# Performance work log

Measured on AMD Instinct MI355X. Metric: run time of the kernel, lower is better.

The kernel has to match this reference:

```python
import jax, jax.numpy as jnp
import numpy as np

B, C, H, W = 64, 256, 14, 14
K = 9
HID = 256   # EdgeAgg hidden_channels = in_channels
OUT = 512   # out_channels = 2*in_channels (required by final reshape)


def _knn(q, kset, k):
    # ViG dense_knn_matrix: squared-distance knn, top-k of -dist (self-loop may be included)
    qs = jnp.sum(q * q, -1)
    ks = jnp.sum(kset * kset, -1)
    dist = qs[:, :, None] - 2.0 * jnp.einsum('bnc,bmc->bnm', q, kset) + ks[:, None, :]
    _, idx = jax.lax.top_k(-dist, k)   # (B,N,k) neighbor indices into kset
    return idx


def _edgeconv_add(feat, nbr, validf, w, b):
    # PyG EdgeConv(nn=Linear, aggr='add') with per-node valid-edge mask:
    #   out[i] = sum_{j in valid nbrs(i)} cat(x_i, x_j - x_i) @ w + b
    # nn is linear, so aggregate neighbor diffs BEFORE the matmul (same math, less traffic).
    Cf = feat.shape[-1]
    wa, wb = w[:Cf], w[Cf:]
    deg = jnp.sum(validf, -1, keepdims=True)                   # (B,N,1)
    xj = feat[jnp.arange(feat.shape[0])[:, None, None], nbr]   # (B,N,k,C) gather
    sum_xj = jnp.einsum('bnkc,bnk->bnc', xj, validf)
    return deg * (feat @ wa + b) + (sum_xj - deg * feat) @ wb


def _forward(x, fc1_w, fc1_b, fc2_w, fc2_b, fce_w, fce_b, inout_w, inout_b,
             attn_w, attn_b, upd_w, upd_b, kp_w, kp_b, enc_w, enc_b,
             mu_w, mu_b, dec_w, dec_b, T):
    k = dec_w.shape[-1]
    b_, c_, h_, w_ = x.shape
    n = h_ * w_
    xs = x.reshape(b_, c_, n)                       # (B,C,N)
    x_sp = jnp.transpose(xs, (0, 2, 1))             # (B,N,C) true spatial node feats for knn
    x_sp_d = jax.lax.stop_gradient(x_sp)            # original detaches before knn
    x_nbr = _knn(x_sp_d, x_sp_d, k)
    # temporal roll across the T frames of each clip
    y_sp = jnp.roll(x_sp.reshape(b_ // T, T, n, c_), -1, axis=1).reshape(b_, n, c_)
    y_nbr = _knn(x_sp_d, jax.lax.stop_gradient(y_sp), k)
    # faithful to original: x.view(B*N, C) reinterprets the contiguous (B,C,N) buffer
    x_feat = xs.reshape(b_, n, c_)
    y_feat = jnp.transpose(y_sp, (0, 2, 1)).reshape(b_, n, c_)
    # VAE-like K predictor (deterministic z = mu); argmax -> per-node degree in [0,k)
    hk = x_feat.reshape(b_ * n, c_) @ kp_w + kp_b
    hk = jax.nn.relu(hk @ enc_w + enc_b)
    mu = hk @ mu_w + mu_b
    logits = mu @ dec_w + dec_b                     # (B*N, k)
    k_int = jnp.argmax(logits, axis=1)
    # generate_mask: keep the first k_int[i] of node i's k edges
    validf = (jnp.arange(k)[None, :] < k_int[:, None]).astype(x.dtype).reshape(b_, n, k)

    def edge_agg(feat, nbr):
        h1 = jax.nn.relu(_edgeconv_add(feat, nbr, validf, fc1_w, fc1_b))
        h2 = _edgeconv_add(h1, nbr, validf, fc2_w, fc2_b)
        return (h2 @ fce_w + fce_b).reshape(b_ * n, -1)

    x_agg = edge_agg(x_feat, x_nbr)
    y_agg = edge_agg(y_feat, y_nbr)
    scores = (jnp.concatenate([x_agg, y_agg], -1) @ attn_w + attn_b)[:, 0]
    wgt = jax.nn.softmax(scores, axis=0)[:, None]   # softmax over ALL B*N nodes (as in source)
    fused = wgt * x_agg + (1.0 - wgt) * y_agg
    xin = x_feat.reshape(b_ * n, c_) @ inout_w + inout_b
    upd = jax.nn.relu(jnp.concatenate([xin, fused], -1) @ upd_w + upd_b)   # (B*N, 2C)
    return jnp.transpose(upd.reshape(b_, n, 2 * c_), (0, 2, 1)).reshape(b_, 2 * c_, h_, w_)


def setup_inputs():
    key = jax.random.key(0)
    ks = iter(jax.random.split(key, 32))

    def lin(i, o):
        return jax.random.normal(next(ks), (i, o), jnp.float32) / np.sqrt(i)

    def bias(o):
        return jax.random.normal(next(ks), (o,), jnp.float32) * 0.01

    return {
        'x': jax.random.normal(next(ks), (B, C, H, W), jnp.float32),
        'fc1_w': lin(2 * C, HID), 'fc1_b': bias(HID),
        'fc2_w': lin(2 * HID, HID), 'fc2_b': bias(HID),
        'fce_w': lin(HID, OUT), 'fce_b': bias(OUT),
        'inout_w': lin(C, OUT), 'inout_b': bias(OUT),
        'attn_w': lin(2 * OUT, 1), 'attn_b': bias(1),
        'upd_w': lin(2 * OUT, OUT), 'upd_b': bias(OUT),
        'kp_w': lin(C, 500), 'kp_b': bias(500),
        'enc_w': lin(500, 64), 'enc_b': bias(64),
        'mu_w': lin(64, 32), 'mu_b': bias(32),
        'dec_w': lin(32, K), 'dec_b': bias(K),
        'T': 16,
    }


def reference(x, fc1_w, fc1_b, fc2_w, fc2_b, fce_w, fce_b, inout_w, inout_b,
              attn_w, attn_b, upd_w, upd_b, kp_w, kp_b, enc_w, enc_b,
              mu_w, mu_b, dec_w, dec_b, T):
    return _forward(x, fc1_w, fc1_b, fc2_w, fc2_b, fce_w, fce_b, inout_w, inout_b,
                    attn_w, attn_b, upd_w, upd_b, kp_w, kp_b, enc_w, enc_b,
                    mu_w, mu_b, dec_w, dec_b, T)
```

## Files before the change

### kernel.cpp

```cpp
#include <hip/hip_runtime.h>
#include <cstddef>
#include <cstdint>

constexpr int BATCH = 64;
constexpr int CH    = 256;
constexpr int NPT   = 196;
constexpr int ROWS  = BATCH * NPT;
constexpr int BSTRIDE = CH * NPT;
constexpr int KNB   = 8;
constexpr int DSTR  = 208;

typedef __bf16 bf16x8 __attribute__((ext_vector_type(8)));
typedef __bf16 bf16x4 __attribute__((ext_vector_type(4)));
typedef _Float16 f16x8 __attribute__((ext_vector_type(8)));
typedef float  f32x4  __attribute__((ext_vector_type(4)));
typedef unsigned long long u64;

__device__ __forceinline__ int src_batch(int b) {
    return (b & ~15) | ((b + 1) & 15);
}

__device__ __forceinline__ void gload_lds16(const void* g, void* l) {
    __builtin_amdgcn_global_load_lds(
        (const __attribute__((address_space(1))) void*)g,
        (__attribute__((address_space(3))) void*)l, 16, 0, 0);
}

__device__ __forceinline__ int xcd_swz(int lin, int nwg) {
    int q = nwg >> 3;
    return (lin & 7) * q + (lin >> 3);
}

__global__ __launch_bounds__(256) void front_kernel(const float* __restrict__ x,
        _Float16* __restrict__ XH, _Float16* __restrict__ XL,
        __bf16* __restrict__ XB, float* __restrict__ qs,
        const float* __restrict__ W1, const float* __restrict__ b1,
        const float* __restrict__ W2, const float* __restrict__ b2,
        int* __restrict__ kint, float* __restrict__ degf) {
    __shared__ __attribute__((aligned(16))) char smem[21056];
    int bid = blockIdx.x;
    int t = threadIdx.x;
    if (bid < 1024) {
        float (*tile)[65] = (float(*)[65])smem;
        int m0 = (bid & 3) * 64, c0 = ((bid >> 2) & 3) * 64, b = bid >> 4;
        const float* xb = x + (size_t)b * BSTRIDE;
        #pragma unroll
        for (int s = 0; s < 16; ++s) {
            int idx = s * 256 + t;
            int cc = idx >> 6, mm = idx & 63;
            int m = m0 + mm;
            float v = (m < NPT) ? xb[(size_t)(c0 + cc) * NPT + m] : 0.f;
            tile[cc][mm] = v;
            if (m < NPT)
                XB[(size_t)b * BSTRIDE + (size_t)(c0 + cc) * NPT + m] = (__bf16)v;
        }
        __syncthreads();
        #pragma unroll
        for (int s = 0; s < 16; ++s) {
            int idx = s * 256 + t;
            int mm = idx >> 6, cc = idx & 63;
            float v = tile[cc][mm];
            _Float16 h = (_Float16)v;
            size_t off = ((size_t)b * 256 + (m0 + mm)) * 256 + c0 + cc;
            XH[off] = h;
            XL[off] = (_Float16)(v - (float)h);
        }
    } else if (bid < 1088) {
        int b = bid - 1024;
        int m = t;
        if (m >= NPT) return;
        const float* xb = x + (size_t)b * BSTRIDE;
        float acc = 0.f;
        for (int c = 0; c < CH; ++c) {
            float v = xb[c * NPT + m];
            acc = fmaf(v, v, acc);
        }
        qs[b * NPT + m] = acc;
    } else {
        float (*xr)[256] = (float(*)[256])smem;
        float (*ebuf)[64] = (float(*)[64])(smem + 16384);
        float (*lg)[9]   = (float(*)[9])(smem + 20480);
        int r0 = (bid - 1088) * 16;
        const float4* xg = (const float4*)(x + (size_t)r0 * 256);
        float4* xs = (float4*)&xr[0][0];
        #pragma unroll
        for (int s = 0; s < 4; ++s) xs[s * 256 + t] = xg[s * 256 + t];
        __syncthreads();
        int w = t >> 6, l = t & 63;
        {
            float bb = b1[l];
            float a0 = bb, a1 = bb, a2 = bb, a3 = bb;
            const float* x0 = xr[w * 4 + 0];
            const float* x1 = xr[w * 4 + 1];
            const float* x2 = xr[w * 4 + 2];
            const float* x3 = xr[w * 4 + 3];
            for (int c = 0; c < 256; ++c) {
                float wv = W1[c * 64 + l];
                a0 = fmaf(x0[c], wv, a0);
                a1 = fmaf(x1[c], wv, a1);
                a2 = fmaf(x2[c], wv, a2);
                a3 = fmaf(x3[c], wv, a3);
            }
            ebuf[w * 4 + 0][l] = fmaxf(a0, 0.f);
            ebuf[w * 4 + 1][l] = fmaxf(a1, 0.f);
            ebuf[w * 4 + 2][l] = fmaxf(a2, 0.f);
            ebuf[w * 4 + 3][l] = fmaxf(a3, 0.f);
        }
        __syncthreads();
        int rr = t >> 4, cc = t & 15;
        if (cc < 9) {
            float acc = b2[cc];
            for (int j = 0; j < 64; ++j)
                acc = fmaf(ebuf[rr][j], W2[j * 9 + cc], acc);
            lg[rr][cc] = acc;
        }
        __syncthreads();
        if (cc == 0) {
            float best = lg[rr][0];
            int bi = 0;
            #pragma unroll
            for (int j = 1; j < 9; ++j)
                if (lg[rr][j] > best) { best = lg[rr][j]; bi = j; }
            kint[r0 + rr] = bi;
            degf[r0 + rr] = (float)bi;
        }
    }
}

__global__ __launch_bounds__(256) void gram_mfma(const _Float16* __restrict__ XH,
        const _Float16* __restrict__ XL, const float* __restrict__ qs,
        float* __restrict__ Dw) {
    __shared__ __attribute__((aligned(16))) _Float16 Ah[128 * 64];
    __shared__ __attribute__((aligned(16))) _Float16 Al[128 * 64];
    __shared__ __attribute__((aligned(16))) _Float16 Bh[128 * 64];
    __shared__ __attribute__((aligned(16))) _Float16 Bl[128 * 64];
    int lin = blockIdx.x + 2 * blockIdx.y + 4 * blockIdx.z;
    int nid = xcd_swz(lin, 512);
    int bx = nid & 1, by = (nid >> 1) & 1;
    int job = nid >> 2;
    int qb = (job < 64) ? job : job - 64;
    int kb = (job < 64) ? qb : src_batch(qb);
    int t = threadIdx.x, w = t >> 6, l = t & 63;
    int r0 = by * 128, c0 = bx * 128;
    int lr = l & 15, lg = l >> 4;
    int wr = (w >> 1) * 64, wc = (w & 1) * 64;
    const _Float16* qh = XH + (size_t)qb * 65536;
    const _Float16* ql = XL + (size_t)qb * 65536;
    const _Float16* kh = XH + (size_t)kb * 65536;
    const _Float16* kl = XL + (size_t)kb * 65536;
    f32x4 acc[4][4] = {};
    for (int k0 = 0; k0 < 256; k0 += 64) {
        #pragma unroll
        for (int i = 0; i < 4; ++i) {
            int row = (w * 4 + i) * 8 + (l >> 3);
            int c8 = l & 7;
            size_t goA = (size_t)(r0 + row) * 256 + k0 + c8 * 8;
            size_t goB = (size_t)(c0 + row) * 256 + k0 + c8 * 8;
            gload_lds16(qh + goA, Ah + (w * 4 + i) * 512);
            gload_lds16(ql + goA, Al + (w * 4 + i) * 512);
            gload_lds16(kh + goB, Bh + (w * 4 + i) * 512);
            gload_lds16(kl + goB, Bl + (w * 4 + i) * 512);
        }
        asm volatile("s_waitcnt vmcnt(0)" ::: "memory");
        __syncthreads();
        #pragma unroll
        for (int ks = 0; ks < 2; ++ks) {
            f16x8 ah[4], al[4], bh[4], bl[4];
            #pragma unroll
            for (int mi = 0; mi < 4; ++mi) {
                ah[mi] = *(const f16x8*)(Ah + (wr + mi * 16 + lr) * 64 + ks * 32 + lg * 8);
                al[mi] = *(const f16x8*)(Al + (wr + mi * 16 + lr) * 64 + ks * 32 + lg * 8);
            }
            #pragma unroll
            for (int ni = 0; ni < 4; ++ni) {
                bh[ni] = *(const f16x8*)(Bh + (wc + ni * 16 + lr) * 64 + ks * 32 + lg * 8);
                bl[ni] = *(const f16x8*)(Bl + (wc + ni * 16 + lr) * 64 + ks * 32 + lg * 8);
            }
            #pragma unroll
            for (int mi = 0; mi < 4; ++mi)
                #pragma unroll
                for (int ni = 0; ni < 4; ++ni) {
                    acc[mi][ni] = __builtin_amdgcn_mfma_f32_16x16x32_f16(
                        ah[mi], bh[ni], acc[mi][ni], 0, 0, 0);
                    acc[mi][ni] = __builtin_amdgcn_mfma_f32_16x16x32_f16(
                        ah[mi], bl[ni], acc[mi][ni], 0, 0, 0);
                    acc[mi][ni] = __builtin_amdgcn_mfma_f32_16x16x32_f16(
                        al[mi], bh[ni], acc[mi][ni], 0, 0, 0);
                }
        }
        __syncthreads();
    }
    const float* qsq = qs + qb * NPT;
    const float* qsk = qs + kb * NPT;
    float ksv[4];
    #pragma unroll
    for (int ni = 0; ni < 4; ++ni) {
        int col = c0 + wc + ni * 16 + lr;
        ksv[ni] = (col < NPT) ? qsk[col] : 0.f;
    }
    #pragma unroll
    for (int mi = 0; mi < 4; ++mi) {
        #pragma unroll
        for (int r = 0; r < 4; ++r) {
            if (r0 + wr + mi * 16 + r >= NPT) continue;
            int grow = r0 + wr + mi * 16 + lg * 4 + r;
            if (grow >= NPT) continue;
            float qq = qsq[grow];
            size_t rbase = ((size_t)job * NPT + grow) * DSTR;
            #pragma unroll
            for (int ni = 0; ni < 4; ++ni) {
                int col = c0 + wc + ni * 16 + lr;
                if (col < NPT)
                    Dw[rbase + col] = qq - 2.f * acc[mi][ni][r] + ksv[ni];
            }
        }
    }
}

__global__ __launch_bounds__(256) void topk_kernel(const float* __restrict__ Dw,
                                                   int* __restrict__ nbr) {
    __shared__ u64 lists[64][4][8];
    int t = threadIdx.x;
    int lrow = t >> 2, q = t & 3;
    int rowid = blockIdx.x * 64 + lrow;
    const float* rp = Dw + (size_t)rowid * DSTR + q * 52;
    u64 kreg[8];
    #pragma unroll
    for (int p = 0; p < 8; ++p) kreg[p] = ~0ull;
    for (int s4 = 0; s4 < 13; ++s4) {
        f32x4 dv = *(const f32x4*)(rp + s4 * 4);
        #pragma unroll
        for (int e = 0; e < 4; ++e) {
            int col = q * 52 + s4 * 4 + e;
            unsigned u = __float_as_uint(dv[e]);
            u = (u & 0x80000000u) ? ~u : (u | 0x80000000u);
            u64 key = (col < NPT) ? (((u64)u << 32) | (unsigned)col) : ~0ull;
            if (key < kreg[7]) {
                #pragma unroll
                for (int p = 0; p < 8; ++p) {
                    u64 mn = (key < kreg[p]) ? key : kreg[p];
                    u64 mx = (key < kreg[p]) ? kreg[p] : key;
                    kreg[p] = mn; key = mx;
                }
            }
        }
    }
    #pragma unroll
    for (int p = 0; p < 8; ++p) lists[lrow][q][p] = kreg[p];
    __syncthreads();
    if (q == 0) {
        const u64* c = &lists[lrow][0][0];
        int p0 = 0, p1 = 0, p2 = 0, p3 = 0;
        #pragma unroll
        for (int it = 0; it < 8; ++it) {
            u64 v0 = c[p0], v1 = c[8 + p1], v2 = c[16 + p2], v3 = c[24 + p3];
            u64 best = v0; int bj = 0;
            if (v1 < best) { best = v1; bj = 1; }
            if (v2 < best) { best = v2; bj = 2; }
            if (v3 < best) { best = v3; bj = 3; }
            if (bj == 0) p0 = (p0 < 7) ? p0 + 1 : 7;
            else if (bj == 1) p1 = (p1 < 7) ? p1 + 1 : 7;
            else if (bj == 2) p2 = (p2 < 7) ? p2 + 1 : 7;
            else p3 = (p3 < 7) ? p3 + 1 : 7;
            nbr[(size_t)rowid * KNB + it] = (int)(best & 0xffffffffu);
        }
    }
}

__global__ __launch_bounds__(256) void prep_weights(
        const float* __restrict__ fc1_w, const float* __restrict__ fc2_w,
        const float* __restrict__ fce_w, const float* __restrict__ upd_w,
        const float* __restrict__ kp_w, const float* __restrict__ kp_b,
        const float* __restrict__ enc_w, const float* __restrict__ enc_b,
        const float* __restrict__ mu_w, const float* __restrict__ mu_b,
        const float* __restrict__ dec_w, const float* __restrict__ dec_b,
        const float* __restrict__ inout_w, const float* __restrict__ inout_b,
        const float* __restrict__ upd_b,
        __bf16* __restrict__ W1catT, __bf16* __restrict__ W2catT,
        __bf16* __restrict__ fcet, __bf16* __restrict__ updC,
        float* __restrict__ KW1, float* __restrict__ kb1,
        float* __restrict__ KW2, float* __restrict__ kb2,
        float* __restrict__ bcomp) {
    __shared__ float tile[64][65];
    int bid = blockIdx.x;
    int t = threadIdx.x;
    if (bid < 64) {
        const float* W = (bid < 32) ? fc1_w : fc2_w;
        __bf16* WT = (bid < 32) ? W1catT : W2catT;
        int local = bid & 31;
        int n0 = (local >> 2) * 64, k0 = (local & 3) * 64;
        #pragma unroll
        for (int s = 0; s < 16; ++s) {
            int idx = s * 256 + t;
            int kk = idx >> 6, nn = idx & 63;
            float v;
            if (n0 < 256)
                v = W[(size_t)(k0 + kk) * 256 + n0 + nn] -
                    W[(size_t)(k0 + kk + 256) * 256 + n0 + nn];
            else
                v = W[(size_t)(k0 + kk + 256) * 256 + (n0 - 256) + nn];
            tile[kk][nn] = v;
        }
        __syncthreads();
        #pragma unroll
        for (int s = 0; s < 16; ++s) {
            int idx = s * 256 + t;
            int nn = idx >> 6, kk = idx & 63;
            WT[(size_t)(n0 + nn) * 256 + k0 + kk] = (__bf16)tile[kk][nn];
        }
    } else if (bid < 96) {
        int local = bid - 64;
        int n0 = (local >> 2) * 64, k0 = (local & 3) * 64;
        #pragma unroll
        for (int s = 0; s < 16; ++s) {
            int idx = s * 256 + t;
            int kk = idx >> 6, nn = idx & 63;
            tile[kk][nn] = fce_w[(size_t)(k0 + kk) * 512 + n0 + nn];
        }
        __syncthreads();
        #pragma unroll
        for (int s = 0; s < 16; ++s) {
            int idx = s * 256 + t;
            int nn = idx >> 6, kk = idx & 63;
            fcet[(size_t)(n0 + nn) * 256 + k0 + kk] = (__bf16)tile[kk][nn];
        }
    } else if (bid < 160) {
        int local = bid - 96;
        int k0 = (local >> 3) * 64, n0 = (local & 7) * 64;
        #pragma unroll
        for (int s = 0; s < 16; ++s) {
            int idx = s * 256 + t;
            int kk = idx >> 6, nn = idx & 63;
            tile[kk][nn] = upd_w[(size_t)(512 + k0 + kk) * 512 + n0 + nn];
        }
        __syncthreads();
        #pragma unroll
        for (int s = 0; s < 16; ++s) {
            int idx = s * 256 + t;
            int nn = idx >> 6, kk = idx & 63;
            updC[(size_t)(n0 + nn) * 768 + 256 + k0 + kk] = (__bf16)tile[kk][nn];
        }
    } else if (bid < 224) {
        int i = (bid - 160) * 4 + (t >> 6);
        int j = t & 63;
        double acc = 0.0;
        for (int k = 0; k < 500; ++k)
            acc += (double)kp_w[(size_t)i * 500 + k] * (double)enc_w[(size_t)k * 64 + j];
        KW1[i * 64 + j] = (float)acc;
    } else if (bid == 224) {
        int j = t;
        if (j < 64) {
            double acc = (double)enc_b[j];
            for (int k = 0; k < 500; ++k)
                acc += (double)kp_b[k] * (double)enc_w[(size_t)k * 64 + j];
            kb1[j] = (float)acc;
        }
    } else if (bid < 228) {
        int e = (bid - 225) * 256 + t;
        if (e < 576) {
            int i = e / 9, j = e - (e / 9) * 9;
            double acc = 0.0;
            for (int k = 0; k < 32; ++k)
                acc += (double)mu_w[(size_t)i * 32 + k] * (double)dec_w[(size_t)k * 9 + j];
            KW2[e] = (float)acc;
        } else if (e < 585) {
            int j = e - 576;
            double acc = (double)dec_b[j];
            for (int k = 0; k < 32; ++k)
                acc += (double)mu_b[k] * (double)dec_w[(size_t)k * 9 + j];
            kb2[j] = (float)acc;
        }
    } else if (bid < 740) {
        int e = (bid - 228) * 256 + t;
        int k = e >> 9, n = e & 511;
        double acc = 0.0;
        for (int j = 0; j < 512; ++j)
            acc += (double)inout_w[(size_t)k * 512 + j] * (double)upd_w[(size_t)j * 512 + n];
        updC[(size_t)n * 768 + k] = (__bf16)(float)acc;
    } else {
        int n = (bid - 740) * 256 + t;
        double acc = (double)upd_b[n];
        for (int j = 0; j < 512; ++j)
            acc += (double)inout_b[j] * (double)upd_w[(size_t)j * 512 + n];
        bcomp[n] = (float)acc;
    }
}

template<int STAGE, int RELU>
__global__ __launch_bounds__(256) void combine_kernel(const __bf16* __restrict__ P,
        const int* __restrict__ nbr, const int* __restrict__ kint_,
        const float* __restrict__ degf, const float* __restrict__ bias,
        __bf16* __restrict__ H) {
    int g = threadIdx.x >> 6, lane = threadIdx.x & 63;
    int nid = xcd_swz(blockIdx.x, 2 * ROWS / 4);
    int r = nid * 4 + g;
    int branch = (r >= ROWS);
    int rr = r - branch * ROWS;
    int b = rr / NPT, i = rr - b * NPT;
    size_t srow, mbase;
    if constexpr (STAGE == 1) {
        int fb = branch ? src_batch(b) : b;
        srow = (size_t)fb * NPT + i;
        mbase = (size_t)fb * NPT;
    } else {
        srow = (size_t)r;
        mbase = (size_t)branch * ROWS + (size_t)b * NPT;
    }
    const int* nb = nbr + (size_t)branch * ((size_t)ROWS * KNB) + (size_t)rr * KNB;
    bf16x4 sv = *(const bf16x4*)(P + srow * 512 + lane * 4);
    float4 bv = *(const float4*)(bias + lane * 4);
    float s0 = 0.f, s1 = 0.f, s2 = 0.f, s3 = 0.f;
    int kk = kint_[rr];
    for (int tt = 0; tt < kk; ++tt) {
        int m = nb[tt];
        bf16x4 v = *(const bf16x4*)(P + (mbase + m) * 512 + 256 + lane * 4);
        s0 += (float)v[0]; s1 += (float)v[1]; s2 += (float)v[2]; s3 += (float)v[3];
    }
    float dg = degf[rr];
    float o0 = fmaf(dg, (float)sv[0] + bv.x, s0);
    float o1 = fmaf(dg, (float)sv[1] + bv.y, s1);
    float o2 = fmaf(dg, (float)sv[2] + bv.z, s2);
    float o3 = fmaf(dg, (float)sv[3] + bv.w, s3);
    if constexpr (RELU) {
        o0 = fmaxf(o0, 0.f); o1 = fmaxf(o1, 0.f);
        o2 = fmaxf(o2, 0.f); o3 = fmaxf(o3, 0.f);
    }
    bf16x4 ov;
    ov[0] = (__bf16)o0; ov[1] = (__bf16)o1; ov[2] = (__bf16)o2; ov[3] = (__bf16)o3;
    *(bf16x4*)(H + (size_t)r * 256 + lane * 4) = ov;
}

template<int FLAGS, int CONCAT>
__global__ __launch_bounds__(256) void mfma_gemm(
    const __bf16* __restrict__ A0, const __bf16* __restrict__ A1,
    const __bf16* __restrict__ WT, const float* __restrict__ bias,
    float* __restrict__ Cf, __bf16* __restrict__ Cb, int K, int N,
    const float* __restrict__ aw, float* __restrict__ scp,
    const float* __restrict__ wgt) {
    constexpr int SMEMB = (FLAGS & 8) ? (128 * 129 * 4) : (2 * 128 * 64 * 2);
    __shared__ __attribute__((aligned(16))) char smem[SMEMB];
    __bf16* As = (__bf16*)smem;
    __bf16* Bs = As + 128 * 64;
    int lin = blockIdx.x + 4 * blockIdx.y;
    int nid = xcd_swz(lin, 4 * gridDim.y);
    int bx = nid & 3, by = nid >> 2;
    int t = threadIdx.x, w = t >> 6, l = t & 63;
    int r0 = by * 128, c0 = bx * 128;
    int lr = l & 15, lg = l >> 4;
    int wr = (w >> 1) * 64, wc = (w & 1) * 64;
    f32x4 acc[4][4] = {};
    for (int k0 = 0; k0 < K; k0 += 64) {
        #pragma unroll
        for (int i = 0; i < 4; ++i) {
            int row = (w * 4 + i) * 8 + (l >> 3);
            int c8 = l & 7;
            if constexpr (CONCAT == 2) {
                if (k0 < 256) {
                    gload_lds16(A0 + (size_t)(r0 + row) * 256 + k0 + c8 * 8,
                                As + (w * 4 + i) * 512);
                } else {
                    int kk2 = k0 - 256 + c8 * 8;
                    size_t gr = (size_t)(r0 + row);
                    bf16x8 xa = *(const bf16x8*)(A1 + gr * 512 + kk2);
                    bf16x8 ya = *(const bf16x8*)(A1 + ((size_t)ROWS + gr) * 512 + kk2);
                    float wv = wgt[gr];
                    bf16x8 mx;
                    #pragma unroll
                    for (int j = 0; j < 8; ++j)
                        mx[j] = (__bf16)(wv * (float)xa[j] + (1.f - wv) * (float)ya[j]);
                    *(bf16x8*)(As + (w * 4 + i) * 512 + l * 8) = mx;
                }
            } else {
                gload_lds16(A0 + (size_t)(r0 + row) * K + k0 + c8 * 8,
                            As + (w * 4 + i) * 512);
            }
            gload_lds16(WT + (size_t)(c0 + row) * K + k0 + c8 * 8,
                        Bs + (w * 4 + i) * 512);
        }
        asm volatile("s_waitcnt vmcnt(0)" ::: "memory");
        __syncthreads();
        #pragma unroll
        for (int ks = 0; ks < 2; ++ks) {
            bf16x8 af[4], bfr[4];
            #pragma unroll
            for (int mi = 0; mi < 4; ++mi)
                af[mi] = *(const bf16x8*)(As + (wr + mi * 16 + lr) * 64 + ks * 32 + lg * 8);
            #pragma unroll
            for (int ni = 0; ni < 4; ++ni)
                bfr[ni] = *(const bf16x8*)(Bs + (wc + ni * 16 + lr) * 64 + ks * 32 + lg * 8);
            #pragma unroll
            for (int mi = 0; mi < 4; ++mi)
                #pragma unroll
                for (int ni = 0; ni < 4; ++ni)
                    acc[mi][ni] = __builtin_amdgcn_mfma_f32_16x16x32_bf16(
                        af[mi], bfr[ni], acc[mi][ni], 0, 0, 0);
        }
        __syncthreads();
    }
    if constexpr ((FLAGS & 8) != 0) {
        float* tile = (float*)smem;
        #pragma unroll
        for (int mi = 0; mi < 4; ++mi)
            #pragma unroll
            for (int r = 0; r < 4; ++r) {
                int rrow = wr + mi * 16 + lg * 4 + r;
                #pragma unroll
                for (int ni = 0; ni < 4; ++ni) {
                    int ccol = wc + ni * 16 + lr;
                    float v = acc[mi][ni][r];
                    if (bias) v += bias[c0 + ccol];
                    if constexpr ((FLAGS & 1) != 0) v = fmaxf(v, 0.f);
                    tile[rrow * 129 + ccol] = v;
                }
            }
        __syncthreads();
        int cc = t >> 6, rr2 = t & 63;
        #pragma unroll
        for (int cs = 0; cs < 128; cs += 4) {
            #pragma unroll
            for (int h = 0; h < 2; ++h) {
                int row = r0 + rr2 + h * 64;
                int bb = row / NPT, ii = row - bb * NPT;
                Cf[((size_t)bb * 512 + (c0 + cc + cs)) * NPT + ii] =
                    tile[(rr2 + h * 64) * 129 + cc + cs];
            }
        }
    } else if constexpr ((FLAGS & 16) != 0) {
        int half = (r0 >= ROWS) ? 1 : 0;
        float ps[4][4] = {};
        #pragma unroll
        for (int mi = 0; mi < 4; ++mi)
            #pragma unroll
            for (int r = 0; r < 4; ++r) {
                int row = r0 + wr + mi * 16 + lg * 4 + r;
                #pragma unroll
                for (int ni = 0; ni < 4; ++ni) {
                    int col = c0 + wc + ni * 16 + lr;
                    float v = acc[mi][ni][r] + bias[col];
                    Cb[(size_t)row * N + col] = (__bf16)v;
                    ps[mi][r] = fmaf(v, aw[half * 512 + col], ps[mi][r]);
                }
            }
        #pragma unroll
        for (int m = 1; m <= 8; m <<= 1)
            #pragma unroll
            for (int mi = 0; mi < 4; ++mi)
                #pragma unroll
                for (int r = 0; r < 4; ++r)
                    ps[mi][r] += __shfl_xor(ps[mi][r], m, 64);
        if (lr == 0) {
            int slot = half * 8 + bx * 2 + (w & 1);
            #pragma unroll
            for (int mi = 0; mi < 4; ++mi)
                #pragma unroll
                for (int r = 0; r < 4; ++r) {
                    int sr = r0 - half * ROWS + wr + mi * 16 + lg * 4 + r;
                    scp[(size_t)slot * ROWS + sr] = ps[mi][r];
                }
        }
    } else {
        #pragma unroll
        for (int mi = 0; mi < 4; ++mi) {
            #pragma unroll
            for (int r = 0; r < 4; ++r) {
                int row = r0 + wr + mi * 16 + lg * 4 + r;
                #pragma unroll
                for (int ni = 0; ni < 4; ++ni) {
                    int col = c0 + wc + ni * 16 + lr;
                    float v = acc[mi][ni][r];
                    if (bias) v += bias[col];
                    if constexpr ((FLAGS & 1) != 0) v = fmaxf(v, 0.f);
                    if constexpr ((FLAGS & 4) != 0)
                        Cb[(size_t)row * N + col] = (__bf16)v;
                    else
                        Cf[(size_t)row * N + col] = v;
                }
            }
        }
    }
}

__global__ __launch_bounds__(256) void softmax_part(const float* __restrict__ scp,
        const float* __restrict__ ab, float* __restrict__ scores,
        float* __restrict__ mpart, float* __restrict__ spart) {
    __shared__ float red[256];
    int t = threadIdx.x;
    int sr = blockIdx.x * 256 + t;
    float s = ab[0];
    #pragma unroll
    for (int i = 0; i < 16; ++i) s += scp[(size_t)i * ROWS + sr];
    scores[sr] = s;
    red[t] = s; __syncthreads();
    for (int off = 128; off; off >>= 1) {
        if (t < off) red[t] = fmaxf(red[t], red[t + off]);
        __syncthreads();
    }
    float mb = red[0]; __syncthreads();
    red[t] = expf(s - mb); __syncthreads();
    for (int off = 128; off; off >>= 1) {
        if (t < off) red[t] += red[t + off];
        __syncthreads();
    }
    if (t == 0) { mpart[blockIdx.x] = mb; spart[blockIdx.x] = red[0]; }
}

__global__ __launch_bounds__(256) void softmax_fin(const float* __restrict__ mpart,
        const float* __restrict__ spart, const float* __restrict__ scores,
        float* __restrict__ wgt) {
    __shared__ float MS[2];
    if (threadIdx.x == 0) {
        float M = mpart[0];
        for (int i = 1; i < 49; ++i) M = fmaxf(M, mpart[i]);
        float S = 0.f;
        for (int i = 0; i < 49; ++i) S += spart[i] * expf(mpart[i] - M);
        MS[0] = M; MS[1] = S;
    }
    __syncthreads();
    float M = MS[0], denom = MS[1];
    for (int i = threadIdx.x; i < ROWS; i += 256)
        wgt[i] = expf(scores[i] - M) / denom;
}

extern "C" void kernel_launch(void* const* d_in, const int* in_sizes, int n_in,
                              void* d_out, int out_size, void* d_ws, size_t ws_size,
                              hipStream_t stream) {
    (void)in_sizes; (void)n_in; (void)out_size; (void)ws_size;
    const float* x       = (const float*)d_in[0];
    const float* fc1_w   = (const float*)d_in[1];
    const float* fc1_b   = (const float*)d_in[2];
    const float* fc2_w   = (const float*)d_in[3];
    const float* fc2_b   = (const float*)d_in[4];
    const float* fce_w   = (const float*)d_in[5];
    const float* fce_b   = (const float*)d_in[6];
    const float* inout_w = (const float*)d_in[7];
    const float* inout_b = (const float*)d_in[8];
    const float* attn_w  = (const float*)d_in[9];
    const float* attn_b  = (const float*)d_in[10];
    const float* upd_w   = (const float*)d_in[11];
    const float* upd_b   = (const float*)d_in[12];
    const float* kp_w    = (const float*)d_in[13];
    const float* kp_b    = (const float*)d_in[14];
    const float* enc_w   = (const float*)d_in[15];
    const float* enc_b   = (const float*)d_in[16];
    const float* mu_w    = (const float*)d_in[17];
    const float* mu_b    = (const float*)d_in[18];
    const float* dec_w   = (const float*)d_in[19];
    const float* dec_b   = (const float*)d_in[20];
    float* out = (float*)d_out;

    char* base = (char*)d_ws;
    size_t o = 0;
    auto alloc = [&](size_t bytes) -> void* {
        void* p = base + o;
        o += (bytes + 255) & ~(size_t)255;
        return p;
    };
    float* qs     = (float*)alloc(ROWS * 4);
    float* degf   = (float*)alloc(ROWS * 4);
    float* scores = (float*)alloc(ROWS * 4);
    float* wgt    = (float*)alloc(ROWS * 4);
    int*   kint   = (int*)  alloc(ROWS * 4);
    float* KW1    = (float*)alloc(256 * 64 * 4);
    float* kb1    = (float*)alloc(64 * 4);
    float* KW2    = (float*)alloc(64 * 9 * 4);
    float* kb2    = (float*)alloc(9 * 4);
    float* bcomp  = (float*)alloc(512 * 4);
    float* scp    = (float*)alloc((size_t)16 * ROWS * 4);
    float* mpart  = (float*)alloc(64 * 4);
    float* spart  = (float*)alloc(64 * 4);
    int*   nbr    = (int*)  alloc((size_t)128 * NPT * KNB * 4);
    char*  regD   = (char*) alloc((size_t)ROWS * 512 * 2);
    __bf16* XB    = (__bf16*)alloc((size_t)ROWS * 256 * 2);
    __bf16* H1    = (__bf16*)alloc((size_t)2 * ROWS * 256 * 2);
    __bf16* H2    = (__bf16*)alloc((size_t)2 * ROWS * 256 * 2);
    char*  regAGG = (char*) alloc((size_t)2 * ROWS * 512 * 4);
    __bf16* W1catT= (__bf16*)alloc((size_t)512 * 256 * 2);
    __bf16* W2catT= (__bf16*)alloc((size_t)512 * 256 * 2);
    __bf16* fcet  = (__bf16*)alloc((size_t)512 * 256 * 2);
    __bf16* updC  = (__bf16*)alloc((size_t)512 * 768 * 2);
    __bf16* P1buf = (__bf16*)regD;
    _Float16* XSPH = (_Float16*)regAGG;
    _Float16* XSPL = XSPH + (size_t)64 * 256 * 256;
    float* Dw     = (float*)(regAGG + (size_t)17 * 1024 * 1024);
    __bf16* P2buf = (__bf16*)regAGG;
    __bf16* AGGb  = (__bf16*)regAGG;
    __bf16* XAGGb = AGGb;

    prep_weights<<<742, 256, 0, stream>>>(fc1_w, fc2_w, fce_w, upd_w,
                                          kp_w, kp_b, enc_w, enc_b,
                                          mu_w, mu_b, dec_w, dec_b,
                                          inout_w, inout_b, upd_b,
                                          W1catT, W2catT, fcet, updC,
                                          KW1, kb1, KW2, kb2, bcomp);
    front_kernel<<<1872, 256, 0, stream>>>(x, XSPH, XSPL, XB, qs,
                                           KW1, kb1, KW2, kb2, kint, degf);

    gram_mfma<<<dim3(2, 2, 128), 256, 0, stream>>>(XSPH, XSPL, qs, Dw);
    topk_kernel<<<392, 256, 0, stream>>>(Dw, nbr);

    mfma_gemm<4, 0><<<dim3(4, 98), 256, 0, stream>>>(
        XB, nullptr, W1catT, nullptr, nullptr, P1buf, 256, 512,
        nullptr, nullptr, nullptr);
    combine_kernel<1, 1><<<2 * ROWS / 4, 256, 0, stream>>>(
        P1buf, nbr, kint, degf, fc1_b, H1);

    mfma_gemm<4, 0><<<dim3(4, 196), 256, 0, stream>>>(
        H1, nullptr, W2catT, nullptr, nullptr, P2buf, 256, 512,
        nullptr, nullptr, nullptr);
    combine_kernel<2, 0><<<2 * ROWS / 4, 256, 0, stream>>>(
        P2buf, nbr, kint, degf, fc2_b, H2);

    mfma_gemm<20, 0><<<dim3(4, 196), 256, 0, stream>>>(
        H2, nullptr, fcet, fce_b, nullptr, AGGb, 256, 512,
        attn_w, scp, nullptr);

    softmax_part<<<49, 256, 0, stream>>>(scp, attn_b, scores, mpart, spart);
    softmax_fin<<<1, 256, 0, stream>>>(mpart, spart, scores, wgt);

    mfma_gemm<9, 2><<<dim3(4, 98), 256, 0, stream>>>(
        XB, XAGGb, updC, bcomp, out, nullptr, 768, 512,
        nullptr, nullptr, wgt);
}
```

Before: 232.0 us.

## Merge weight prep into front kernel, fuse K-predictor into gram, fold softmax finalize

Moves the weight preparation blocks into the front kernel as extra block ranges, and moves the K-predictor MLP from the front kernel into the gram kernel as extra blocks so it runs after the precomputed weights exist. The gram tile K-step shrinks from 64 to 32 to cut LDS use to 32KB. The two-kernel softmax becomes a single kernel where the last block, found with an atomic counter, computes the final weights. The aim is fewer launches and more overlap across independent work. The cost is a smaller gram K-tile with more syncs, plus last-block atomic synchronisation.

```diff
diff --git a/kernel.cpp b/kernel.cpp
--- a/kernel.cpp
+++ b/kernel.cpp
@@ -34,14 +34,24 @@
 __global__ __launch_bounds__(256) void front_kernel(const float* __restrict__ x,
         _Float16* __restrict__ XH, _Float16* __restrict__ XL,
         __bf16* __restrict__ XB, float* __restrict__ qs,
-        const float* __restrict__ W1, const float* __restrict__ b1,
-        const float* __restrict__ W2, const float* __restrict__ b2,
-        int* __restrict__ kint, float* __restrict__ degf) {
-    __shared__ __attribute__((aligned(16))) char smem[21056];
+        const float* __restrict__ fc1_w, const float* __restrict__ fc2_w,
+        const float* __restrict__ fce_w, const float* __restrict__ upd_w,
+        const float* __restrict__ kp_w, const float* __restrict__ kp_b,
+        const float* __restrict__ enc_w, const float* __restrict__ enc_b,
+        const float* __restrict__ mu_w, const float* __restrict__ mu_b,
+        const float* __restrict__ dec_w, const float* __restrict__ dec_b,
+        const float* __restrict__ inout_w, const float* __restrict__ inout_b,
+        const float* __restrict__ upd_b,
+        __bf16* __restrict__ W1catT, __bf16* __restrict__ W2catT,
+        __bf16* __restrict__ fcet, __bf16* __restrict__ updC,
+        float* __restrict__ KW1, float* __restrict__ kb1,
+        float* __restrict__ KW2, float* __restrict__ kb2,
+        float* __restrict__ bcomp, int* __restrict__ smcnt) {
+    __shared__ __attribute__((aligned(16))) char smem[16896];
+    float (*tile)[65] = (float(*)[65])smem;
     int bid = blockIdx.x;
     int t = threadIdx.x;
     if (bid < 1024) {
-        float (*tile)[65] = (float(*)[65])smem;
         int m0 = (bid & 3) * 64, c0 = ((bid >> 2) & 3) * 64, b = bid >> 4;
         const float* xb = x + (size_t)b * BSTRIDE;
         #pragma unroll
@@ -77,10 +87,211 @@
         }
         qs[b * NPT + m] = acc;
     } else {
+        int pbid = bid - 1088;
+        if (pbid == 0 && t == 0) smcnt[0] = 0;
+        if (pbid < 64) {
+            const float* W = (pbid < 32) ? fc1_w : fc2_w;
+            __bf16* WT = (pbid < 32) ? W1catT : W2catT;
+            int local = pbid & 31;
+            int n0 = (local >> 2) * 64, k0 = (local & 3) * 64;
+            #pragma unroll
+            for (int s = 0; s < 16; ++s) {
+                int idx = s * 256 + t;
+                int kk = idx >> 6, nn = idx & 63;
+                float v;
+                if (n0 < 256)
+                    v = W[(size_t)(k0 + kk) * 256 + n0 + nn] -
+                        W[(size_t)(k0 + kk + 256) * 256 + n0 + nn];
+                else
+                    v = W[(size_t)(k0 + kk + 256) * 256 + (n0 - 256) + nn];
+                tile[kk][nn] = v;
+            }
+            __syncthreads();
+            #pragma unroll
+            for (int s = 0; s < 16; ++s) {
+                int idx = s * 256 + t;
+                int nn = idx >> 6, kk = idx & 63;
+                WT[(size_t)(n0 + nn) * 256 + k0 + kk] = (__bf16)tile[kk][nn];
+            }
+        } else if (pbid < 96) {
+            int local = pbid - 64;
+            int n0 = (local >> 2) * 64, k0 = (local & 3) * 64;
+            #pragma unroll
+            for (int s = 0; s < 16; ++s) {
+                int idx = s * 256 + t;
+                int kk = idx >> 6, nn = idx & 63;
+                tile[kk][nn] = fce_w[(size_t)(k0 + kk) * 512 + n0 + nn];
+            }
+            __syncthreads();
+            #pragma unroll
+            for (int s = 0; s < 16; ++s) {
+                int idx = s * 256 + t;
+                int nn = idx >> 6, kk = idx & 63;
+                fcet[(size_t)(n0 + nn) * 256 + k0 + kk] = (__bf16)tile[kk][nn];
+            }
+        } else if (pbid < 160) {
+            int local = pbid - 96;
+            int k0 = (local >> 3) * 64, n0 = (local & 7) * 64;
+            #pragma unroll
+            for (int s = 0; s < 16; ++s) {
+                int idx = s * 256 + t;
+                int kk = idx >> 6, nn = idx & 63;
+                tile[kk][nn] = upd_w[(size_t)(512 + k0 + kk) * 512 + n0 + nn];
+            }
+            __syncthreads();
+            #pragma unroll
+            for (int s = 0; s < 16; ++s) {
+                int idx = s * 256 + t;
+                int nn = idx >> 6, kk = idx & 63;
+                updC[(size_t)(n0 + nn) * 768 + 256 + k0 + kk] = (__bf16)tile[kk][nn];
+            }
+        } else if (pbid < 224) {
+            int i = (pbid - 160) * 4 + (t >> 6);
+            int j = t & 63;
+            double acc = 0.0;
+            for (int k = 0; k < 500; ++k)
+                acc += (double)kp_w[(size_t)i * 500 + k] * (double)enc_w[(size_t)k * 64 + j];
+            KW1[i * 64 + j] = (float)acc;
+        } else if (pbid == 224) {
+            int j = t;
+            if (j < 64) {
+                double acc = (double)enc_b[j];
+                for (int k = 0; k < 500; ++k)
+                    acc += (double)kp_b[k] * (double)enc_w[(size_t)k * 64 + j];
+                kb1[j] = (float)acc;
+            }
+        } else if (pbid < 228) {
+            int e = (pbid - 225) * 256 + t;
+            if (e < 576) {
+                int i = e / 9, j = e - (e / 9) * 9;
+                double acc = 0.0;
+                for (int k = 0; k < 32; ++k)
+                    acc += (double)mu_w[(size_t)i * 32 + k] * (double)dec_w[(size_t)k * 9 + j];
+                KW2[e] = (float)acc;
+            } else if (e < 585) {
+                int j = e - 576;
+                double acc = (double)dec_b[j];
+                for (int k = 0; k < 32; ++k)
+                    acc += (double)mu_b[k] * (double)dec_w[(size_t)k * 9 + j];
+                kb2[j] = (float)acc;
+            }
+        } else if (pbid < 740) {
+            int e = (pbid - 228) * 256 + t;
+            int k = e >> 9, n = e & 511;
+            double acc = 0.0;
+            for (int j = 0; j < 512; ++j)
+                acc += (double)inout_w[(size_t)k * 512 + j] * (double)upd_w[(size_t)j * 512 + n];
+            updC[(size_t)n * 768 + k] = (__bf16)(float)acc;
+        } else {
+            int n = (pbid - 740) * 256 + t;
+            double acc = (double)upd_b[n];
+            for (int j = 0; j < 512; ++j)
+                acc += (double)inout_b[j] * (double)upd_w[(size_t)j * 512 + n];
+            bcomp[n] = (float)acc;
+        }
+    }
+}
+
+__global__ __launch_bounds__(256) void gram_kint(const _Float16* __restrict__ XH,
+        const _Float16* __restrict__ XL, const float* __restrict__ qs,
+        float* __restrict__ Dw, const float* __restrict__ x,
+        const float* __restrict__ W1, const float* __restrict__ b1,
+        const float* __restrict__ W2, const float* __restrict__ b2,
+        int* __restrict__ kint, float* __restrict__ degf) {
+    __shared__ __attribute__((aligned(16))) char smem[32768];
+    int bid = blockIdx.x;
+    int t = threadIdx.x;
+    if (bid < 512) {
+        _Float16* Ah = (_Float16*)smem;
+        _Float16* Al = Ah + 4096;
+        _Float16* Bh = Al + 4096;
+        _Float16* Bl = Bh + 4096;
+        int nid = xcd_swz(bid, 512);
+        int bx = nid & 1, by = (nid >> 1) & 1;
+        int job = nid >> 2;
+        int qb = (job < 64) ? job : job - 64;
+        int kb = (job < 64) ? qb : src_batch(qb);
+        int w = t >> 6, l = t & 63;
+        int r0 = by * 128, c0 = bx * 128;
+        int lr = l & 15, lg = l >> 4;
+        int wr = (w >> 1) * 64, wc = (w & 1) * 64;
+        const _Float16* qh = XH + (size_t)qb * 65536;
+        const _Float16* ql = XL + (size_t)qb * 65536;
+        const _Float16* kh = XH + (size_t)kb * 65536;
+        const _Float16* kl = XL + (size_t)kb * 65536;
+        f32x4 acc[4][4] = {};
+        for (int k0 = 0; k0 < 256; k0 += 32) {
+            #pragma unroll
+            for (int i = 0; i < 2; ++i) {
+                int row = w * 32 + i * 16 + (l >> 2);
+                int c8 = (l & 3) * 8;
+                size_t goA = (size_t)(r0 + row) * 256 + k0 + c8;
+                size_t goB = (size_t)(c0 + row) * 256 + k0 + c8;
+                _Float16* dA = Ah + w * 1024 + i * 512;
+                _Float16* dAl = Al + w * 1024 + i * 512;
+                _Float16* dB = Bh + w * 1024 + i * 512;
+                _Float16* dBl = Bl + w * 1024 + i * 512;
+                gload_lds16(qh + goA, dA);
+                gload_lds16(ql + goA, dAl);
+                gload_lds16(kh + goB, dB);
+                gload_lds16(kl + goB, dBl);
+            }
+            asm volatile("s_waitcnt vmcnt(0)" ::: "memory");
+            __syncthreads();
+            f16x8 ah[4], alv[4], bh[4], blv[4];
+            #pragma unroll
+            for (int mi = 0; mi < 4; ++mi) {
+                ah[mi]  = *(const f16x8*)(Ah + (wr + mi * 16 + lr) * 32 + lg * 8);
+                alv[mi] = *(const f16x8*)(Al + (wr + mi * 16 + lr) * 32 + lg * 8);
+            }
+            #pragma unroll
+            for (int ni = 0; ni < 4; ++ni) {
+                bh[ni]  = *(const f16x8*)(Bh + (wc + ni * 16 + lr) * 32 + lg * 8);
+                blv[ni] = *(const f16x8*)(Bl + (wc + ni * 16 + lr) * 32 + lg * 8);
+            }
+            #pragma unroll
+            for (int mi = 0; mi < 4; ++mi)
+                #pragma unroll
+                for (int ni = 0; ni < 4; ++ni) {
+                    acc[mi][ni] = __builtin_amdgcn_mfma_f32_16x16x32_f16(
+                        ah[mi], bh[ni], acc[mi][ni], 0, 0, 0);
+                    acc[mi][ni] = __builtin_amdgcn_mfma_f32_16x16x32_f16(
+                        ah[mi], blv[ni], acc[mi][ni], 0, 0, 0);
+                    acc[mi][ni] = __builtin_amdgcn_mfma_f32_16x16x32_f16(
+                        alv[mi], bh[ni], acc[mi][ni], 0, 0, 0);
+                }
+            __syncthreads();
+        }
+        const float* qsq = qs + qb * NPT;
+        const float* qsk = qs + kb * NPT;
+        float ksv[4];
+        #pragma unroll
+        for (int ni = 0; ni < 4; ++ni) {
+            int col = c0 + wc + ni * 16 + lr;
+            ksv[ni] = (col < NPT) ? qsk[col] : 0.f;
+        }
+        #pragma unroll
+        for (int mi = 0; mi < 4; ++mi) {
+            #pragma unroll
+            for (int r = 0; r < 4; ++r) {
+                if (r0 + wr + mi * 16 + r >= NPT) continue;
+                int grow = r0 + wr + mi * 16 + lg * 4 + r;
+                if (grow >= NPT) continue;
+                float qq = qsq[grow];
+                size_t rbase = ((size_t)job * NPT + grow) * DSTR;
+                #pragma unroll
+                for (int ni = 0; ni < 4; ++ni) {
+                    int col = c0 + wc + ni * 16 + lr;
+                    if (col < NPT)
+                        Dw[rbase + col] = qq - 2.f * acc[mi][ni][r] + ksv[ni];
+                }
+            }
+        }
+    } else {
         float (*xr)[256] = (float(*)[256])smem;
         float (*ebuf)[64] = (float(*)[64])(smem + 16384);
-        float (*lg)[9]   = (float(*)[9])(smem + 20480);
-        int r0 = (bid - 1088) * 16;
+        float (*lg2)[9]  = (float(*)[9])(smem + 20480);
+        int r0 = (bid - 512) * 16;
         const float4* xg = (const float4*)(x + (size_t)r0 * 256);
         float4* xs = (float4*)&xr[0][0];
         #pragma unroll
@@ -112,107 +323,17 @@
             float acc = b2[cc];
             for (int j = 0; j < 64; ++j)
                 acc = fmaf(ebuf[rr][j], W2[j * 9 + cc], acc);
-            lg[rr][cc] = acc;
+            lg2[rr][cc] = acc;
         }
         __syncthreads();
         if (cc == 0) {
-            float best = lg[rr][0];
+            float best = lg2[rr][0];
             int bi = 0;
             #pragma unroll
             for (int j = 1; j < 9; ++j)
-                if (lg[rr][j] > best) { best = lg[rr][j]; bi = j; }
+                if (lg2[rr][j] > best) { best = lg2[rr][j]; bi = j; }
             kint[r0 + rr] = bi;
             degf[r0 + rr] = (float)bi;
-        }
-    }
-}
-
-__global__ __launch_bounds__(256) void gram_mfma(const _Float16* __restrict__ XH,
-        const _Float16* __restrict__ XL, const float* __restrict__ qs,
-        float* __restrict__ Dw) {
-    __shared__ __attribute__((aligned(16))) _Float16 Ah[128 * 64];
-    __shared__ __attribute__((aligned(16))) _Float16 Al[128 * 64];
-    __shared__ __attribute__((aligned(16))) _Float16 Bh[128 * 64];
-    __shared__ __attribute__((aligned(16))) _Float16 Bl[128 * 64];
-    int lin = blockIdx.x + 2 * blockIdx.y + 4 * blockIdx.z;
-    int nid = xcd_swz(lin, 512);
-    int bx = nid & 1, by = (nid >> 1) & 1;
-    int job = nid >> 2;
-    int qb = (job < 64) ? job : job - 64;
-    int kb = (job < 64) ? qb : src_batch(qb);
-    int t = threadIdx.x, w = t >> 6, l = t & 63;
-    int r0 = by * 128, c0 = bx * 128;
-    int lr = l & 15, lg = l >> 4;
-    int wr = (w >> 1) * 64, wc = (w & 1) * 64;
-    const _Float16* qh = XH + (size_t)qb * 65536;
-    const _Float16* ql = XL + (size_t)qb * 65536;
-    const _Float16* kh = XH + (size_t)kb * 65536;
-    const _Float16* kl = XL + (size_t)kb * 65536;
-    f32x4 acc[4][4] = {};
-    for (int k0 = 0; k0 < 256; k0 += 64) {
-        #pragma unroll
-        for (int i = 0; i < 4; ++i) {
-            int row = (w * 4 + i) * 8 + (l >> 3);
-            int c8 = l & 7;
-            size_t goA = (size_t)(r0 + row) * 256 + k0 + c8 * 8;
-            size_t goB = (size_t)(c0 + row) * 256 + k0 + c8 * 8;
-            gload_lds16(qh + goA, Ah + (w * 4 + i) * 512);
-            gload_lds16(ql + goA, Al + (w * 4 + i) * 512);
-            gload_lds16(kh + goB, Bh + (w * 4 + i) * 512);
-            gload_lds16(kl + goB, Bl + (w * 4 + i) * 512);
-        }
-        asm volatile("s_waitcnt vmcnt(0)" ::: "memory");
-        __syncthreads();
-        #pragma unroll
-        for (int ks = 0; ks < 2; ++ks) {
-            f16x8 ah[4], al[4], bh[4], bl[4];
-            #pragma unroll
-            for (int mi = 0; mi < 4; ++mi) {
-                ah[mi] = *(const f16x8*)(Ah + (wr + mi * 16 + lr) * 64 + ks * 32 + lg * 8);
-                al[mi] = *(const f16x8*)(Al + (wr + mi * 16 + lr) * 64 + ks * 32 + lg * 8);
-            }
-            #pragma unroll
-            for (int ni = 0; ni < 4; ++ni) {
-                bh[ni] = *(const f16x8*)(Bh + (wc + ni * 16 + lr) * 64 + ks * 32 + lg * 8);
-                bl[ni] = *(const f16x8*)(Bl + (wc + ni * 16 + lr) * 64 + ks * 32 + lg * 8);
-            }
-            #pragma unroll
-            for (int mi = 0; mi < 4; ++mi)
-                #pragma unroll
-                for (int ni = 0; ni < 4; ++ni) {
-                    acc[mi][ni] = __builtin_amdgcn_mfma_f32_16x16x32_f16(
-                        ah[mi], bh[ni], acc[mi][ni], 0, 0, 0);
-                    acc[mi][ni] = __builtin_amdgcn_mfma_f32_16x16x32_f16(
-                        ah[mi], bl[ni], acc[mi][ni], 0, 0, 0);
-                    acc[mi][ni] = __builtin_amdgcn_mfma_f32_16x16x32_f16(
-                        al[mi], bh[ni], acc[mi][ni], 0, 0, 0);
-                }
-        }
-        __syncthreads();
-    }
-    const float* qsq = qs + qb * NPT;
-    const float* qsk = qs + kb * NPT;
-    float ksv[4];
-    #pragma unroll
-    for (int ni = 0; ni < 4; ++ni) {
-        int col = c0 + wc + ni * 16 + lr;
-        ksv[ni] = (col < NPT) ? qsk[col] : 0.f;
-    }
-    #pragma unroll
-    for (int mi = 0; mi < 4; ++mi) {
-        #pragma unroll
-        for (int r = 0; r < 4; ++r) {
-            if (r0 + wr + mi * 16 + r >= NPT) continue;
-            int grow = r0 + wr + mi * 16 + lg * 4 + r;
-            if (grow >= NPT) continue;
-            float qq = qsq[grow];
-            size_t rbase = ((size_t)job * NPT + grow) * DSTR;
-            #pragma unroll
-            for (int ni = 0; ni < 4; ++ni) {
-                int col = c0 + wc + ni * 16 + lr;
-                if (col < NPT)
-                    Dw[rbase + col] = qq - 2.f * acc[mi][ni][r] + ksv[ni];
-            }
         }
     }
 }
@@ -264,125 +385,6 @@
             else p3 = (p3 < 7) ? p3 + 1 : 7;
             nbr[(size_t)rowid * KNB + it] = (int)(best & 0xffffffffu);
         }
-    }
-}
-
-__global__ __launch_bounds__(256) void prep_weights(
-        const float* __restrict__ fc1_w, const float* __restrict__ fc2_w,
-        const float* __restrict__ fce_w, const float* __restrict__ upd_w,
-        const float* __restrict__ kp_w, const float* __restrict__ kp_b,
-        const float* __restrict__ enc_w, const float* __restrict__ enc_b,
-        const float* __restrict__ mu_w, const float* __restrict__ mu_b,
-        const float* __restrict__ dec_w, const float* __restrict__ dec_b,
-        const float* __restrict__ inout_w, const float* __restrict__ inout_b,
-        const float* __restrict__ upd_b,
-        __bf16* __restrict__ W1catT, __bf16* __restrict__ W2catT,
-        __bf16* __restrict__ fcet, __bf16* __restrict__ updC,
-        float* __restrict__ KW1, float* __restrict__ kb1,
-        float* __restrict__ KW2, float* __restrict__ kb2,
-        float* __restrict__ bcomp) {
-    __shared__ float tile[64][65];
-    int bid = blockIdx.x;
-    int t = threadIdx.x;
-    if (bid < 64) {
-        const float* W = (bid < 32) ? fc1_w : fc2_w;
-        __bf16* WT = (bid < 32) ? W1catT : W2catT;
-        int local = bid & 31;
-        int n0 = (local >> 2) * 64, k0 = (local & 3) * 64;
-        #pragma unroll
-        for (int s = 0; s < 16; ++s) {
-            int idx = s * 256 + t;
-            int kk = idx >> 6, nn = idx & 63;
-            float v;
-            if (n0 < 256)
-                v = W[(size_t)(k0 + kk) * 256 + n0 + nn] -
-                    W[(size_t)(k0 + kk + 256) * 256 + n0 + nn];
-            else
-                v = W[(size_t)(k0 + kk + 256) * 256 + (n0 - 256) + nn];
-            tile[kk][nn] = v;
-        }
-        __syncthreads();
-        #pragma unroll
-        for (int s = 0; s < 16; ++s) {
-            int idx = s * 256 + t;
-            int nn = idx >> 6, kk = idx & 63;
-            WT[(size_t)(n0 + nn) * 256 + k0 + kk] = (__bf16)tile[kk][nn];
-        }
-    } else if (bid < 96) {
-        int local = bid - 64;
-        int n0 = (local >> 2) * 64, k0 = (local & 3) * 64;
-        #pragma unroll
-        for (int s = 0; s < 16; ++s) {
-            int idx = s * 256 + t;
-            int kk = idx >> 6, nn = idx & 63;
-            tile[kk][nn] = fce_w[(size_t)(k0 + kk) * 512 + n0 + nn];
-        }
-        __syncthreads();
-        #pragma unroll
-        for (int s = 0; s < 16; ++s) {
-            int idx = s * 256 + t;
-            int nn = idx >> 6, kk = idx & 63;
-            fcet[(size_t)(n0 + nn) * 256 + k0 + kk] = (__bf16)tile[kk][nn];
-        }
-    } else if (bid < 160) {
-        int local = bid - 96;
-        int k0 = (local >> 3) * 64, n0 = (local & 7) * 64;
-        #pragma unroll
-        for (int s = 0; s < 16; ++s) {
-            int idx = s * 256 + t;
-            int kk = idx >> 6, nn = idx & 63;
-            tile[kk][nn] = upd_w[(size_t)(512 + k0 + kk) * 512 + n0 + nn];
-        }
-        __syncthreads();
-        #pragma unroll
-        for (int s = 0; s < 16; ++s) {
-            int idx = s * 256 + t;
-            int nn = idx >> 6, kk = idx & 63;
-            updC[(size_t)(n0 + nn) * 768 + 256 + k0 + kk] = (__bf16)tile[kk][nn];
-        }
-    } else if (bid < 224) {
-        int i = (bid - 160) * 4 + (t >> 6);
-        int j = t & 63;
-        double acc = 0.0;
-        for (int k = 0; k < 500; ++k)
-            acc += (double)kp_w[(size_t)i * 500 + k] * (double)enc_w[(size_t)k * 64 + j];
-        KW1[i * 64 + j] = (float)acc;
-    } else if (bid == 224) {
-        int j = t;
-        if (j < 64) {
-            double acc = (double)enc_b[j];
-            for (int k = 0; k < 500; ++k)
-                acc += (double)kp_b[k] * (double)enc_w[(size_t)k * 64 + j];
-            kb1[j] = (float)acc;
-        }
-    } else if (bid < 228) {
-        int e = (bid - 225) * 256 + t;
-        if (e < 576) {
-            int i = e / 9, j = e - (e / 9) * 9;
-            double acc = 0.0;
-            for (int k = 0; k < 32; ++k)
-                acc += (double)mu_w[(size_t)i * 32 + k] * (double)dec_w[(size_t)k * 9 + j];
-            KW2[e] = (float)acc;
-        } else if (e < 585) {
-            int j = e - 576;
-            double acc = (double)dec_b[j];
-            for (int k = 0; k < 32; ++k)
-                acc += (double)mu_b[k] * (double)dec_w[(size_t)k * 9 + j];
-            kb2[j] = (float)acc;
-        }
-    } else if (bid < 740) {
-        int e = (bid - 228) * 256 + t;
-        int k = e >> 9, n = e & 511;
-        double acc = 0.0;
-        for (int j = 0; j < 512; ++j)
-            acc += (double)inout_w[(size_t)k * 512 + j] * (double)upd_w[(size_t)j * 512 + n];
-        updC[(size_t)n * 768 + k] = (__bf16)(float)acc;
-    } else {
-        int n = (bid - 740) * 256 + t;
-        double acc = (double)upd_b[n];
-        for (int j = 0; j < 512; ++j)
-            acc += (double)inout_b[j] * (double)upd_w[(size_t)j * 512 + n];
-        bcomp[n] = (float)acc;
     }
 }
 
@@ -580,10 +582,13 @@
     }
 }
 
-__global__ __launch_bounds__(256) void softmax_part(const float* __restrict__ scp,
+__global__ __launch_bounds__(256) void softmax_all(const float* __restrict__ scp,
         const float* __restrict__ ab, float* __restrict__ scores,
-        float* __restrict__ mpart, float* __restrict__ spart) {
+        float* __restrict__ mpart, float* __restrict__ spart,
+        int* __restrict__ cnt, float* __restrict__ wgt) {
     __shared__ float red[256];
+    __shared__ float MS[2];
+    __shared__ bool islast;
     int t = threadIdx.x;
     int sr = blockIdx.x * 256 + t;
     float s = ab[0];
@@ -601,23 +606,27 @@
         if (t < off) red[t] += red[t + off];
         __syncthreads();
     }
-    if (t == 0) { mpart[blockIdx.x] = mb; spart[blockIdx.x] = red[0]; }
-}
-
-__global__ __launch_bounds__(256) void softmax_fin(const float* __restrict__ mpart,
-        const float* __restrict__ spart, const float* __restrict__ scores,
-        float* __restrict__ wgt) {
-    __shared__ float MS[2];
-    if (threadIdx.x == 0) {
+    if (t == 0) {
+        mpart[blockIdx.x] = mb;
+        spart[blockIdx.x] = red[0];
+        __threadfence();
+        int old = atomicAdd(cnt, 1);
+        islast = (old == 48);
+    }
+    __syncthreads();
+    if (!islast) return;
+    __threadfence();
+    if (t == 0) {
         float M = mpart[0];
         for (int i = 1; i < 49; ++i) M = fmaxf(M, mpart[i]);
         float S = 0.f;
         for (int i = 0; i < 49; ++i) S += spart[i] * expf(mpart[i] - M);
         MS[0] = M; MS[1] = S;
+        cnt[0] = 0;
     }
     __syncthreads();
     float M = MS[0], denom = MS[1];
-    for (int i = threadIdx.x; i < ROWS; i += 256)
+    for (int i = t; i < ROWS; i += 256)
         wgt[i] = expf(scores[i] - M) / denom;
 }
 
@@ -668,6 +677,7 @@
     float* scp    = (float*)alloc((size_t)16 * ROWS * 4);
     float* mpart  = (float*)alloc(64 * 4);
     float* spart  = (float*)alloc(64 * 4);
+    int*   smcnt  = (int*)  alloc(256);
     int*   nbr    = (int*)  alloc((size_t)128 * NPT * KNB * 4);
     char*  regD   = (char*) alloc((size_t)ROWS * 512 * 2);
     __bf16* XB    = (__bf16*)alloc((size_t)ROWS * 256 * 2);
@@ -686,16 +696,16 @@
     __bf16* AGGb  = (__bf16*)regAGG;
     __bf16* XAGGb = AGGb;
 
-    prep_weights<<<742, 256, 0, stream>>>(fc1_w, fc2_w, fce_w, upd_w,
-                                          kp_w, kp_b, enc_w, enc_b,
-                                          mu_w, mu_b, dec_w, dec_b,
-                                          inout_w, inout_b, upd_b,
-                                          W1catT, W2catT, fcet, updC,
-                                          KW1, kb1, KW2, kb2, bcomp);
-    front_kernel<<<1872, 256, 0, stream>>>(x, XSPH, XSPL, XB, qs,
-                                           KW1, kb1, KW2, kb2, kint, degf);
-
-    gram_mfma<<<dim3(2, 2, 128), 256, 0, stream>>>(XSPH, XSPL, qs, Dw);
+    front_kernel<<<1830, 256, 0, stream>>>(x, XSPH, XSPL, XB, qs,
+                                           fc1_w, fc2_w, fce_w, upd_w,
+                                           kp_w, kp_b, enc_w, enc_b,
+                                           mu_w, mu_b, dec_w, dec_b,
+                                           inout_w, inout_b, upd_b,
+                                           W1catT, W2catT, fcet, updC,
+                                           KW1, kb1, KW2, kb2, bcomp, smcnt);
+
+    gram_kint<<<1296, 256, 0, stream>>>(XSPH, XSPL, qs, Dw, x,
+                                        KW1, kb1, KW2, kb2, kint, degf);
     topk_kernel<<<392, 256, 0, stream>>>(Dw, nbr);
 
     mfma_gemm<4, 0><<<dim3(4, 98), 256, 0, stream>>>(
@@ -714,8 +724,8 @@
         H2, nullptr, fcet, fce_b, nullptr, AGGb, 256, 512,
         attn_w, scp, nullptr);
 
-    softmax_part<<<49, 256, 0, stream>>>(scp, attn_b, scores, mpart, spart);
-    softmax_fin<<<1, 256, 0, stream>>>(mpart, spart, scores, wgt);
+    softmax_all<<<49, 256, 0, stream>>>(scp, attn_b, scores, mpart, spart,
+                                        smcnt, wgt);
 
     mfma_gemm<9, 2><<<dim3(4, 98), 256, 0, stream>>>(
         XB, XAGGb, updC, bcomp, out, nullptr, 768, 512,
```

Measured after the change: 232.0 us. No clear change (-0.0%).
